# Kernel optimization log

Measured on AMD Instinct MI355X. Metric: run time of the kernel, lower is better.

## Reference

```python
import jax, jax.numpy as jnp
import numpy as np

N, A, D_IN, H, S = 4096, 256, 39, 50, 8


def setup_inputs() -> dict:
    key = jax.random.key(0)
    ks = jax.random.split(key, 8)
    sc1 = 1.0 / np.sqrt(D_IN)
    sc2 = 1.0 / np.sqrt(H)
    return {
        "desc": jax.random.normal(ks[0], (N, A, D_IN), dtype=jnp.float32),
        "numbers": jax.random.randint(ks[1], (A,), 0, S),
        "W1": jax.random.normal(ks[2], (S, D_IN, H), dtype=jnp.float32) * sc1,
        "b1": jax.random.normal(ks[3], (S, H), dtype=jnp.float32) * sc1,
        "W2": jax.random.normal(ks[4], (S, H, H), dtype=jnp.float32) * sc2,
        "b2": jax.random.normal(ks[5], (S, H), dtype=jnp.float32) * sc2,
        "W3": jax.random.normal(ks[6], (S, H, 1), dtype=jnp.float32) * sc2,
        "b3": jax.random.normal(ks[7], (S, 1), dtype=jnp.float32) * sc2,
    }


def reference(desc, numbers, W1, b1, W2, b2, W3, b3):
    # Species-routed per-atom MLP dispatch, vectorized by gathering each
    # atom's expert parameters (replaces the Python loop over ModuleDict).
    w1 = W1[numbers]            # [A, D_IN, H]
    w2 = W2[numbers]            # [A, H, H]
    w3 = W3[numbers]            # [A, H, 1]
    h = jax.nn.silu(jnp.einsum('nad,adh->nah', desc, w1) + b1[numbers])
    h = jax.nn.silu(jnp.einsum('nah,ahk->nak', h, w2) + b2[numbers])
    out = jnp.einsum('nah,aho->nao', h, w3) + b3[numbers]
    return out[..., 0]          # [N, A], matches tc.cat(temp, axis=1)
```

## Files before the change

### kernel.cpp

```cpp
#include <hip/hip_runtime.h>
#include <hip/hip_bf16.h>
#include <cstring>


#define NN    4096
#define AA    256
#define DIN   39
#define HH    50
#define ATILE 4
#define NTILE 64
#define XSTR  72
#define WFS   (2 * 2 * 4 * 64 * 8)

typedef __attribute__((ext_vector_type(8))) short bf16x8;
typedef __attribute__((ext_vector_type(4))) float f32x4;
typedef float f32x4u __attribute__((ext_vector_type(4), aligned(4)));

__device__ __forceinline__ float fast_silu(float x) {
    return x * __builtin_amdgcn_rcpf(1.0f + __expf(-x));
}
__device__ __forceinline__ unsigned pack_bf2(float a, float b) {
    __hip_bfloat162 h = __float22bfloat162_rn(float2{a, b});
    unsigned u; memcpy(&u, &h, 4); return u;
}
__device__ __forceinline__ bf16x8 cvt8(f32x4u a, f32x4u b) {
    unsigned u[4];
    u[0] = pack_bf2(a[0], a[1]);
    u[1] = pack_bf2(a[2], a[3]);
    u[2] = pack_bf2(b[0], b[1]);
    u[3] = pack_bf2(b[2], b[3]);
    bf16x8 r; memcpy(&r, u, 16); return r;
}

__global__ __launch_bounds__(256) void prep_weights(
    const float* __restrict__ W1, const float* __restrict__ b1,
    const float* __restrict__ W2, const float* __restrict__ b2,
    const float* __restrict__ W3, const float* __restrict__ b3,
    unsigned short* __restrict__ Wf, float* __restrict__ Bp)
{
    const int s = blockIdx.x >> 3;
    const int c = blockIdx.x & 7;
    const int t = threadIdx.x;
    const float* __restrict__ w1g = W1 + s * (DIN * HH);
    const float* __restrict__ w2g = W2 + s * (HH * HH);
    unsigned* __restrict__ outw = (unsigned*)(Wf + (size_t)s * WFS);

    #pragma unroll
    for (int i = 0; i < 2; ++i) {
        const int d    = c * 512 + i * 256 + t;
        const int j2   = d & 3;
        const int lane = (d >> 2) & 63;
        const int mt   = (d >> 8) & 3;
        const int ks   = (d >> 10) & 1;
        const int L    = (d >> 11) & 1;
        const int col  = 16 * mt + (lane & 15);
        const int k0   = ks * 32 + 8 * (lane >> 4) + 2 * j2;
        const int k1   = k0 + 1;
        float v0 = 0.f, v1 = 0.f;
        if (col < HH) {
            if (L == 0) {
                if (k0 < DIN) v0 = w1g[k0 * HH + col];
                if (k1 < DIN) v1 = w1g[k1 * HH + col];
            } else {
                if (k0 < HH)  v0 = w2g[k0 * HH + col];
                if (k1 < HH)  v1 = w2g[k1 * HH + col];
            }
        }
        outw[d] = pack_bf2(v0, v1);
    }
    if (c == 0 && t < 64) {
        float* bp = Bp + s * 256;
        const bool v = t < HH;
        bp[t]       = v ? b1[s * HH + t] : 0.0f;
        bp[64 + t]  = v ? b2[s * HH + t] : 0.0f;
        bp[128 + t] = v ? W3[s * HH + t] : 0.0f;
        bp[192 + t] = b3[s];
    }
}

__global__ __launch_bounds__(256, 4) void atomic_mlp_mfma(
    const float* __restrict__ desc,
    const int*   __restrict__ numbers,
    const unsigned short* __restrict__ Wf,
    const float* __restrict__ Bp,
    float*       __restrict__ out)
{
    __shared__ unsigned short Hb[ATILE * NTILE * XSTR];
    __shared__ float          Ob[ATILE * NTILE];

    const int a0 = blockIdx.x * ATILE;
    const int n0 = blockIdx.y * NTILE;
    const int t  = threadIdx.x;
    const int lane = t & 63;
    const int lg   = lane >> 4;
    const int lr   = lane & 15;
    const int wid  = t >> 6;
    const int wbase = wid * NTILE;

    const int sw = __builtin_amdgcn_readfirstlane(numbers[a0 + wid]);
    const unsigned short* __restrict__ wfs = Wf + (size_t)sw * WFS;
    const float* __restrict__ bp = Bp + sw * 256;

    bf16x8 w1f[2][4];
    #pragma unroll
    for (int ks = 0; ks < 2; ++ks)
        #pragma unroll
        for (int mt = 0; mt < 4; ++mt)
            w1f[ks][mt] = *(const bf16x8*)&wfs[((ks * 4 + mt) * 64 + lane) * 8];
    f32x4 b1q[4];
    #pragma unroll
    for (int mt = 0; mt < 4; ++mt)
        b1q[mt] = *(const f32x4*)&bp[16 * mt + 4 * lg];
    #pragma unroll
    for (int ks = 0; ks < 2; ++ks)
        #pragma unroll
        for (int mt = 0; mt < 4; ++mt)
            asm volatile("" : "+v"(w1f[ks][mt]));
    #pragma unroll
    for (int mt = 0; mt < 4; ++mt) asm volatile("" : "+v"(b1q[mt]));

    const float bias3 = bp[192];

    const size_t arow = (size_t)(a0 + wid) * DIN;
    #pragma unroll
    for (int nt = 0; nt < 4; ++nt) {
        const size_t rbase = (size_t)(n0 + 16 * nt + lr) * (AA * DIN) + arow;
        const f32x4u xa = *(const f32x4u*)(desc + rbase + 8 * lg);
        const f32x4u xb = *(const f32x4u*)(desc + rbase + 8 * lg + 4);
        const f32x4u xc = *(const f32x4u*)(desc + rbase + 32);
        const f32x4u xv = *(const f32x4u*)(desc + rbase + 35);
        f32x4u xd;
        xd[0] = xv[1]; xd[1] = xv[2]; xd[2] = xv[3]; xd[3] = xv[0];
        const bf16x8 xf0 = cvt8(xa, xb);
        const bf16x8 xf1 = cvt8(xc, xd);
        #pragma unroll
        for (int mt = 0; mt < 4; ++mt) {
            f32x4 c = b1q[mt];
            c = __builtin_amdgcn_mfma_f32_16x16x32_bf16(w1f[0][mt], xf0, c, 0, 0, 0);
            c = __builtin_amdgcn_mfma_f32_16x16x32_bf16(w1f[1][mt], xf1, c, 0, 0, 0);
            const unsigned u0 = pack_bf2(fast_silu(c[0]), fast_silu(c[1]));
            unsigned u1;
            if (mt == 3) u1 = 0u;
            else         u1 = pack_bf2(fast_silu(c[2]), fast_silu(c[3]));
            uint2 uu; uu.x = u0; uu.y = u1;
            *(uint2*)&Hb[(wbase + 16 * nt + lr) * XSTR + 16 * mt + 4 * lg] = uu;
        }
    }

    bf16x8 w2f[2][4];
    #pragma unroll
    for (int ks = 0; ks < 2; ++ks)
        #pragma unroll
        for (int mt = 0; mt < 4; ++mt)
            w2f[ks][mt] = *(const bf16x8*)&wfs[((8 + ks * 4 + mt) * 64 + lane) * 8];
    f32x4 b2q[4], w3q[4];
    #pragma unroll
    for (int mt = 0; mt < 4; ++mt) {
        b2q[mt] = *(const f32x4*)&bp[64 + 16 * mt + 4 * lg];
        w3q[mt] = *(const f32x4*)&bp[128 + 16 * mt + 4 * lg];
    }
    #pragma unroll
    for (int ks = 0; ks < 2; ++ks)
        #pragma unroll
        for (int mt = 0; mt < 4; ++mt)
            asm volatile("" : "+v"(w2f[ks][mt]));
    #pragma unroll
    for (int mt = 0; mt < 4; ++mt) {
        asm volatile("" : "+v"(b2q[mt]));
        asm volatile("" : "+v"(w3q[mt]));
    }

    #pragma unroll
    for (int nt = 0; nt < 4; ++nt) {
        const int row = wbase + 16 * nt + lr;
        const bf16x8 hf0 = *(const bf16x8*)&Hb[row * XSTR + 8 * lg];
        const bf16x8 hf1 = *(const bf16x8*)&Hb[row * XSTR + 32 + 8 * lg];
        float p = 0.f;
        #pragma unroll
        for (int mt = 0; mt < 4; ++mt) {
            f32x4 c = b2q[mt];
            c = __builtin_amdgcn_mfma_f32_16x16x32_bf16(w2f[0][mt], hf0, c, 0, 0, 0);
            c = __builtin_amdgcn_mfma_f32_16x16x32_bf16(w2f[1][mt], hf1, c, 0, 0, 0);
            p += fast_silu(c[0]) * w3q[mt][0];
            p += fast_silu(c[1]) * w3q[mt][1];
            if (mt < 3) {
                p += fast_silu(c[2]) * w3q[mt][2];
                p += fast_silu(c[3]) * w3q[mt][3];
            }
        }
        p += __shfl_xor(p, 16);
        p += __shfl_xor(p, 32);
        if (lg == 0) Ob[row] = p + bias3;
    }

    __syncthreads();

    if (t < NTILE) {
        float4 o;
        o.x = Ob[0 * NTILE + t];
        o.y = Ob[1 * NTILE + t];
        o.z = Ob[2 * NTILE + t];
        o.w = Ob[3 * NTILE + t];
        *(float4*)&out[(size_t)(n0 + t) * AA + a0] = o;
    }
}

extern "C" void kernel_launch(void* const* d_in, const int* in_sizes, int n_in,
                              void* d_out, int out_size, void* d_ws, size_t ws_size,
                              hipStream_t stream) {
    const float* desc    = (const float*)d_in[0];
    const int*   numbers = (const int*)  d_in[1];
    const float* W1      = (const float*)d_in[2];
    const float* b1      = (const float*)d_in[3];
    const float* W2      = (const float*)d_in[4];
    const float* b2      = (const float*)d_in[5];
    const float* W3      = (const float*)d_in[6];
    const float* b3      = (const float*)d_in[7];
    float*       out     = (float*)d_out;

    unsigned short* Wf = (unsigned short*)d_ws;
    float*          Bp = (float*)((char*)d_ws + 8 * WFS * 2);

    hipLaunchKernelGGL(prep_weights, dim3(64), dim3(256), 0, stream,
                       W1, b1, W2, b2, W3, b3, Wf, Bp);

    dim3 grid(AA / ATILE, NN / NTILE);
    hipLaunchKernelGGL(atomic_mlp_mfma, grid, dim3(256), 0, stream,
                       desc, numbers, Wf, Bp, out);
}
```

Baseline: 61.48 us.

## Loop each block over several row tiles, keeping expert weights resident in registers

```diff
diff --git a/kernel.cpp b/kernel.cpp
--- a/kernel.cpp
+++ b/kernel.cpp
@@ -9,6 +9,7 @@
 #define HH    50
 #define ATILE 4
 #define NTILE 64
+#define RT    4
 #define XSTR  72
 #define WFS   (2 * 2 * 4 * 64 * 8)
 
@@ -78,7 +79,7 @@
     }
 }
 
-__global__ __launch_bounds__(256, 4) void atomic_mlp_mfma(
+__global__ __launch_bounds__(256, 3) void atomic_mlp_mfma(
     const float* __restrict__ desc,
     const int*   __restrict__ numbers,
     const unsigned short* __restrict__ Wf,
@@ -86,10 +87,9 @@
     float*       __restrict__ out)
 {
     __shared__ unsigned short Hb[ATILE * NTILE * XSTR];
-    __shared__ float          Ob[ATILE * NTILE];
 
     const int a0 = blockIdx.x * ATILE;
-    const int n0 = blockIdx.y * NTILE;
+    const int nb = blockIdx.y * (NTILE * RT);
     const int t  = threadIdx.x;
     const int lane = t & 63;
     const int lg   = lane >> 4;
@@ -101,107 +101,89 @@
     const unsigned short* __restrict__ wfs = Wf + (size_t)sw * WFS;
     const float* __restrict__ bp = Bp + sw * 256;
 
-    bf16x8 w1f[2][4];
+    bf16x8 w1f[2][4], w2f[2][4];
     #pragma unroll
     for (int ks = 0; ks < 2; ++ks)
         #pragma unroll
-        for (int mt = 0; mt < 4; ++mt)
+        for (int mt = 0; mt < 4; ++mt) {
             w1f[ks][mt] = *(const bf16x8*)&wfs[((ks * 4 + mt) * 64 + lane) * 8];
-    f32x4 b1q[4];
-    #pragma unroll
-    for (int mt = 0; mt < 4; ++mt)
+            w2f[ks][mt] = *(const bf16x8*)&wfs[((8 + ks * 4 + mt) * 64 + lane) * 8];
+        }
+    f32x4 b1q[4], b2q[4], w3q[4];
+    #pragma unroll
+    for (int mt = 0; mt < 4; ++mt) {
         b1q[mt] = *(const f32x4*)&bp[16 * mt + 4 * lg];
-    #pragma unroll
-    for (int ks = 0; ks < 2; ++ks)
-        #pragma unroll
-        for (int mt = 0; mt < 4; ++mt)
-            asm volatile("" : "+v"(w1f[ks][mt]));
-    #pragma unroll
-    for (int mt = 0; mt < 4; ++mt) asm volatile("" : "+v"(b1q[mt]));
-
-    const float bias3 = bp[192];
-
-    const size_t arow = (size_t)(a0 + wid) * DIN;
-    #pragma unroll
-    for (int nt = 0; nt < 4; ++nt) {
-        const size_t rbase = (size_t)(n0 + 16 * nt + lr) * (AA * DIN) + arow;
-        const f32x4u xa = *(const f32x4u*)(desc + rbase + 8 * lg);
-        const f32x4u xb = *(const f32x4u*)(desc + rbase + 8 * lg + 4);
-        const f32x4u xc = *(const f32x4u*)(desc + rbase + 32);
-        const f32x4u xv = *(const f32x4u*)(desc + rbase + 35);
-        f32x4u xd;
-        xd[0] = xv[1]; xd[1] = xv[2]; xd[2] = xv[3]; xd[3] = xv[0];
-        const bf16x8 xf0 = cvt8(xa, xb);
-        const bf16x8 xf1 = cvt8(xc, xd);
-        #pragma unroll
-        for (int mt = 0; mt < 4; ++mt) {
-            f32x4 c = b1q[mt];
-            c = __builtin_amdgcn_mfma_f32_16x16x32_bf16(w1f[0][mt], xf0, c, 0, 0, 0);
-            c = __builtin_amdgcn_mfma_f32_16x16x32_bf16(w1f[1][mt], xf1, c, 0, 0, 0);
-            const unsigned u0 = pack_bf2(fast_silu(c[0]), fast_silu(c[1]));
-            unsigned u1;
-            if (mt == 3) u1 = 0u;
-            else         u1 = pack_bf2(fast_silu(c[2]), fast_silu(c[3]));
-            uint2 uu; uu.x = u0; uu.y = u1;
-            *(uint2*)&Hb[(wbase + 16 * nt + lr) * XSTR + 16 * mt + 4 * lg] = uu;
-        }
-    }
-
-    bf16x8 w2f[2][4];
-    #pragma unroll
-    for (int ks = 0; ks < 2; ++ks)
-        #pragma unroll
-        for (int mt = 0; mt < 4; ++mt)
-            w2f[ks][mt] = *(const bf16x8*)&wfs[((8 + ks * 4 + mt) * 64 + lane) * 8];
-    f32x4 b2q[4], w3q[4];
-    #pragma unroll
-    for (int mt = 0; mt < 4; ++mt) {
         b2q[mt] = *(const f32x4*)&bp[64 + 16 * mt + 4 * lg];
         w3q[mt] = *(const f32x4*)&bp[128 + 16 * mt + 4 * lg];
     }
     #pragma unroll
     for (int ks = 0; ks < 2; ++ks)
         #pragma unroll
-        for (int mt = 0; mt < 4; ++mt)
+        for (int mt = 0; mt < 4; ++mt) {
+            asm volatile("" : "+v"(w1f[ks][mt]));
             asm volatile("" : "+v"(w2f[ks][mt]));
+        }
     #pragma unroll
     for (int mt = 0; mt < 4; ++mt) {
+        asm volatile("" : "+v"(b1q[mt]));
         asm volatile("" : "+v"(b2q[mt]));
         asm volatile("" : "+v"(w3q[mt]));
     }
-
-    #pragma unroll
-    for (int nt = 0; nt < 4; ++nt) {
-        const int row = wbase + 16 * nt + lr;
-        const bf16x8 hf0 = *(const bf16x8*)&Hb[row * XSTR + 8 * lg];
-        const bf16x8 hf1 = *(const bf16x8*)&Hb[row * XSTR + 32 + 8 * lg];
-        float p = 0.f;
-        #pragma unroll
-        for (int mt = 0; mt < 4; ++mt) {
-            f32x4 c = b2q[mt];
-            c = __builtin_amdgcn_mfma_f32_16x16x32_bf16(w2f[0][mt], hf0, c, 0, 0, 0);
-            c = __builtin_amdgcn_mfma_f32_16x16x32_bf16(w2f[1][mt], hf1, c, 0, 0, 0);
-            p += fast_silu(c[0]) * w3q[mt][0];
-            p += fast_silu(c[1]) * w3q[mt][1];
-            if (mt < 3) {
-                p += fast_silu(c[2]) * w3q[mt][2];
-                p += fast_silu(c[3]) * w3q[mt][3];
+    const float bias3 = bp[192];
+
+    const size_t arow = (size_t)(a0 + wid) * DIN;
+
+    for (int rt = 0; rt < RT; ++rt) {
+        const int n0 = nb + NTILE * rt;
+
+        #pragma unroll
+        for (int nt = 0; nt < 4; ++nt) {
+            const size_t rbase = (size_t)(n0 + 16 * nt + lr) * (AA * DIN) + arow;
+            const f32x4u xa = *(const f32x4u*)(desc + rbase + 8 * lg);
+            const f32x4u xb = *(const f32x4u*)(desc + rbase + 8 * lg + 4);
+            const f32x4u xc = *(const f32x4u*)(desc + rbase + 32);
+            const f32x4u xv = *(const f32x4u*)(desc + rbase + 35);
+            f32x4u xd;
+            xd[0] = xv[1]; xd[1] = xv[2]; xd[2] = xv[3]; xd[3] = xv[0];
+            const bf16x8 xf0 = cvt8(xa, xb);
+            const bf16x8 xf1 = cvt8(xc, xd);
+            #pragma unroll
+            for (int mt = 0; mt < 4; ++mt) {
+                f32x4 c = b1q[mt];
+                c = __builtin_amdgcn_mfma_f32_16x16x32_bf16(w1f[0][mt], xf0, c, 0, 0, 0);
+                c = __builtin_amdgcn_mfma_f32_16x16x32_bf16(w1f[1][mt], xf1, c, 0, 0, 0);
+                const unsigned u0 = pack_bf2(fast_silu(c[0]), fast_silu(c[1]));
+                unsigned u1;
+                if (mt == 3) u1 = 0u;
+                else         u1 = pack_bf2(fast_silu(c[2]), fast_silu(c[3]));
+                uint2 uu; uu.x = u0; uu.y = u1;
+                *(uint2*)&Hb[(wbase + 16 * nt + lr) * XSTR + 16 * mt + 4 * lg] = uu;
             }
         }
-        p += __shfl_xor(p, 16);
-        p += __shfl_xor(p, 32);
-        if (lg == 0) Ob[row] = p + bias3;
-    }
-
-    __syncthreads();
-
-    if (t < NTILE) {
-        float4 o;
-        o.x = Ob[0 * NTILE + t];
-        o.y = Ob[1 * NTILE + t];
-        o.z = Ob[2 * NTILE + t];
-        o.w = Ob[3 * NTILE + t];
-        *(float4*)&out[(size_t)(n0 + t) * AA + a0] = o;
+
+        #pragma unroll
+        for (int nt = 0; nt < 4; ++nt) {
+            const int row = wbase + 16 * nt + lr;
+            const bf16x8 hf0 = *(const bf16x8*)&Hb[row * XSTR + 8 * lg];
+            const bf16x8 hf1 = *(const bf16x8*)&Hb[row * XSTR + 32 + 8 * lg];
+            float p = 0.f;
+            #pragma unroll
+            for (int mt = 0; mt < 4; ++mt) {
+                f32x4 c = b2q[mt];
+                c = __builtin_amdgcn_mfma_f32_16x16x32_bf16(w2f[0][mt], hf0, c, 0, 0, 0);
+                c = __builtin_amdgcn_mfma_f32_16x16x32_bf16(w2f[1][mt], hf1, c, 0, 0, 0);
+                p += fast_silu(c[0]) * w3q[mt][0];
+                p += fast_silu(c[1]) * w3q[mt][1];
+                if (mt < 3) {
+                    p += fast_silu(c[2]) * w3q[mt][2];
+                    p += fast_silu(c[3]) * w3q[mt][3];
+                }
+            }
+            p += __shfl_xor(p, 16);
+            p += __shfl_xor(p, 32);
+            if (lg == 0)
+                out[(size_t)(n0 + 16 * nt + lr) * AA + (a0 + wid)] = p + bias3;
+        }
     }
 }
 
@@ -224,7 +206,7 @@
     hipLaunchKernelGGL(prep_weights, dim3(64), dim3(256), 0, stream,
                        W1, b1, W2, b2, W3, b3, Wf, Bp);
 
-    dim3 grid(AA / ATILE, NN / NTILE);
+    dim3 grid(AA / ATILE, NN / (NTILE * RT));
     hipLaunchKernelGGL(atomic_mlp_mfma, grid, dim3(256), 0, stream,
                        desc, numbers, Wf, Bp, out);
 }
```

Result: slower. 62.81 us (+2.2%).
